# Optimization experiments

Hardware: AMD Instinct MI355X
Metric: run time of the kernel (lower is better)

## Reference

```python
import jax, jax.numpy as jnp
import numpy as np

HIDDEN = 9000
EMBED = 300
STEPS = 20


def _lstm_cell(x, h, c, w_ih, w_hh, b_ih, b_hh):
    # x: [1, in], h/c: [1, H]; gates: [1, 4H] in torch order i, f, g, o
    gates = x @ w_ih.T + b_ih + h @ w_hh.T + b_hh
    i, f, g, o = jnp.split(gates, 4, axis=-1)
    c_new = jax.nn.sigmoid(f) * c + jax.nn.sigmoid(i) * jnp.tanh(g)
    h_new = jax.nn.sigmoid(o) * jnp.tanh(c_new)
    return h_new, c_new


def setup_inputs() -> dict:
    key = jax.random.key(0)
    ks = jax.random.split(key, 7)
    s = 1.0 / np.sqrt(HIDDEN)  # torch LSTMCell/Linear default init scale
    x = jax.random.normal(ks[0], (1, EMBED), dtype=jnp.float32)
    w_ih = jax.random.uniform(ks[1], (4 * HIDDEN, EMBED), jnp.float32, -s, s)
    w_hh = jax.random.uniform(ks[2], (4 * HIDDEN, HIDDEN), jnp.float32, -s, s)
    b_ih = jax.random.uniform(ks[3], (4 * HIDDEN,), jnp.float32, -s, s)
    b_hh = jax.random.uniform(ks[4], (4 * HIDDEN,), jnp.float32, -s, s)
    w_out = jax.random.uniform(ks[5], (EMBED, HIDDEN), jnp.float32, -s, s)
    b_out = jax.random.uniform(ks[6], (EMBED,), jnp.float32, -s, s)
    return {"x": x, "w_ih": w_ih, "w_hh": w_hh, "b_ih": b_ih,
            "b_hh": b_hh, "w_out": w_out, "b_out": b_out}


def reference(x, w_ih, w_hh, b_ih, b_hh, w_out, b_out):
    h = jnp.zeros((1, HIDDEN), dtype=x.dtype)
    c = jnp.zeros((1, HIDDEN), dtype=x.dtype)
    # priming step: feed the image/word embedding once
    h, c = _lstm_cell(x, h, c, w_ih, w_hh, b_ih, b_hh)

    def step(carry, _):
        h, c = carry
        out = h @ w_out.T + b_out          # [1, EMBED]
        h, c = _lstm_cell(out, h, c, w_ih, w_hh, b_ih, b_hh)
        h = jax.nn.softmax(h, axis=1)      # softmax over hidden dim, as in source
        return (h, c), h[0]

    (_, _), hs = jax.lax.scan(step, (h, c), None, length=STEPS)
    return hs.T  # [HIDDEN, STEPS] == gen_cap[:, 1:]
```

## Files before the change

### kernel.cpp

```cpp
#include <hip/hip_runtime.h>
#include <hip/hip_fp16.h>
#include <math.h>

#define HID 9000
#define EMB 300
#define NSTEPS 20
#define RS 9216
#define HID8 1125
#define EMB4 75
#define F4_ROW 2250
#define QROW_DW 1152
#define QHALF 576
#define Q_D    1.4054567378526131e-3f
#define Q_INVD 711.5124735378853f

__device__ __forceinline__ float sigmoidf_(float v) {
    return 1.0f / (1.0f + expf(-v));
}

__device__ __forceinline__ float waveReduceSum(float v) {
#pragma unroll
    for (int off = 32; off > 0; off >>= 1) v += __shfl_down(v, off, 64);
    return v;
}

#define I4DOT8(d, v0, v1, aA, aB)                                      \
    {   unsigned int _d = (d);                                         \
        aA = fmaf((float)(((int)(_d << 28)) >> 28), v0.x, aA);         \
        aB = fmaf((float)(((int)(_d << 24)) >> 28), v0.y, aB);         \
        aA = fmaf((float)(((int)(_d << 20)) >> 28), v0.z, aA);         \
        aB = fmaf((float)(((int)(_d << 16)) >> 28), v0.w, aB);         \
        aA = fmaf((float)(((int)(_d << 12)) >> 28), v1.x, aA);         \
        aB = fmaf((float)(((int)(_d <<  8)) >> 28), v1.y, aB);         \
        aA = fmaf((float)(((int)(_d <<  4)) >> 28), v1.z, aA);         \
        aB = fmaf((float)(((int)(_d      )) >> 28), v1.w, aB); }

__device__ __forceinline__ unsigned int quant4(float v) {
    int q = (int)rintf(v * Q_INVD);
    q = q < -8 ? -8 : (q > 7 ? 7 : q);
    return (unsigned int)(q & 0xF);
}

__global__ __launch_bounds__(256) void f32_to_f16_kernel(
    const float* __restrict__ src, __half* __restrict__ dst, int n8)
{
    int i = blockIdx.x * blockDim.x + threadIdx.x;
    const int stride = gridDim.x * blockDim.x;
    const float4* __restrict__ s4 = (const float4*)src;
    float4* __restrict__ d4 = (float4*)dst;
    for (; i < n8; i += stride) {
        float4 a = s4[2 * i];
        float4 b = s4[2 * i + 1];
        float4 o;
        ((__half2*)&o)[0] = __floats2half2_rn(a.x, a.y);
        ((__half2*)&o)[1] = __floats2half2_rn(a.z, a.w);
        ((__half2*)&o)[2] = __floats2half2_rn(b.x, b.y);
        ((__half2*)&o)[3] = __floats2half2_rn(b.z, b.w);
        d4[i] = o;
    }
}

__global__ __launch_bounds__(256) void prime_kernel_h(
    const float* __restrict__ x, const __half* __restrict__ w_ih,
    const float* __restrict__ b_ih, const float* __restrict__ b_hh,
    float* __restrict__ h, float* __restrict__ c, float* __restrict__ hist)
{
    const int j = blockIdx.x;
    const int wave = threadIdx.x >> 6;
    const int lane = threadIdx.x & 63;
    const int row = j + wave * HID;
    const float2* __restrict__ wr = (const float2*)(w_ih + (size_t)row * EMB);
    const float4* __restrict__ x4 = (const float4*)x;
    float acc = 0.0f;
    for (int k = lane; k < EMB4; k += 64) {
        float2 wv = wr[k];
        const __half2* wh = (const __half2*)&wv;
        float2 w0 = __half22float2(wh[0]);
        float2 w1 = __half22float2(wh[1]);
        float4 xv = x4[k];
        acc = fmaf(w0.x, xv.x, acc);
        acc = fmaf(w0.y, xv.y, acc);
        acc = fmaf(w1.x, xv.z, acc);
        acc = fmaf(w1.y, xv.w, acc);
    }
    acc = waveReduceSum(acc);
    __shared__ float gl[4];
    if (lane == 0) gl[wave] = acc + b_ih[row] + b_hh[row];
    __syncthreads();
    if (threadIdx.x == 0) {
        float gi = gl[0], gg = gl[2], go = gl[3];
        float cn = sigmoidf_(gi) * tanhf(gg);
        float hn = sigmoidf_(go) * tanhf(cn);
        c[j] = cn;
        h[j] = hn;
    }
    if (blockIdx.x == 0 && threadIdx.x < RS - HID) h[HID + threadIdx.x] = 0.0f;
    if (blockIdx.x >= 1 && blockIdx.x <= NSTEPS && threadIdx.x < RS - HID)
        hist[(size_t)(blockIdx.x - 1) * RS + HID + threadIdx.x] = 0.0f;
}

__global__ __launch_bounds__(256) void outvec_kernel_h(
    const float* __restrict__ h, const __half* __restrict__ w_out,
    const float* __restrict__ b_out, float* __restrict__ ovec, float sOverride)
{
    const int i = blockIdx.x;
    const float4* __restrict__ wr = (const float4*)(w_out + (size_t)i * HID);
    const float4* __restrict__ h4 = (const float4*)h;
    const bool selfS = sOverride <= 0.0f;
    float acc = 0.0f, se = 0.0f;
    for (int k = threadIdx.x; k < HID8; k += 256) {
        float4 wv = wr[k];
        const __half2* wh = (const __half2*)&wv;
        float4 ha = h4[2 * k];
        float4 hb = h4[2 * k + 1];
        if (selfS)
            se += ((ha.x + ha.y) + (ha.z + ha.w)) + ((hb.x + hb.y) + (hb.z + hb.w));
        float2 w0 = __half22float2(wh[0]);
        float2 w1 = __half22float2(wh[1]);
        float2 w2 = __half22float2(wh[2]);
        float2 w3 = __half22float2(wh[3]);
        acc = fmaf(w0.x, ha.x, acc);
        acc = fmaf(w0.y, ha.y, acc);
        acc = fmaf(w1.x, ha.z, acc);
        acc = fmaf(w1.y, ha.w, acc);
        acc = fmaf(w2.x, hb.x, acc);
        acc = fmaf(w2.y, hb.y, acc);
        acc = fmaf(w3.x, hb.z, acc);
        acc = fmaf(w3.y, hb.w, acc);
    }
    acc = waveReduceSum(acc);
    se = waveReduceSum(se);
    __shared__ float r1[4], r2[4];
    const int wave = threadIdx.x >> 6;
    const int lane = threadIdx.x & 63;
    if (lane == 0) { r1[wave] = acc; r2[wave] = se; }
    __syncthreads();
    if (threadIdx.x == 0) {
        float S = selfS ? ((r2[0] + r2[1]) + (r2[2] + r2[3])) : sOverride;
        ovec[i] = ((r1[0] + r1[1]) + (r1[2] + r1[3])) / S + b_out[i];
    }
}

__global__ __launch_bounds__(256) void convgates_q4(
    const float* __restrict__ h, const float* __restrict__ ovec,
    const float* __restrict__ w_hh, unsigned int* __restrict__ whh4,
    const __half* __restrict__ w_ih,
    const float* __restrict__ b_ih, const float* __restrict__ b_hh,
    float* __restrict__ c, float* __restrict__ e_out)
{
    const int j = blockIdx.x;
    const int wave = threadIdx.x >> 6;
    const int lane = threadIdx.x & 63;
    const int row = j + wave * HID;

    const float4* __restrict__ w4 = (const float4*)(w_hh + (size_t)row * HID);
    unsigned int* __restrict__ dst = whh4 + (size_t)row * QROW_DW;
    const float4* __restrict__ h4 = (const float4*)h;
    float acc = 0.0f;
    for (int it = 0; it < 18; ++it) {
        const int ci = it * 64 + lane;
        unsigned int pack = 0u;
        if (ci < HID8) {
            float4 a = w4[2 * ci];
            float4 b = w4[2 * ci + 1];
            float4 ha = h4[2 * ci];
            float4 hb = h4[2 * ci + 1];
            acc = fmaf(a.x, ha.x, acc);
            acc = fmaf(a.y, ha.y, acc);
            acc = fmaf(a.z, ha.z, acc);
            acc = fmaf(a.w, ha.w, acc);
            acc = fmaf(b.x, hb.x, acc);
            acc = fmaf(b.y, hb.y, acc);
            acc = fmaf(b.z, hb.z, acc);
            acc = fmaf(b.w, hb.w, acc);
            pack = quant4(a.x)
                 | (quant4(a.y) << 4)
                 | (quant4(a.z) << 8)
                 | (quant4(a.w) << 12)
                 | (quant4(b.x) << 16)
                 | (quant4(b.y) << 20)
                 | (quant4(b.z) << 24)
                 | (quant4(b.w) << 28);
        }
        dst[ci] = pack;
    }
    const float2* __restrict__ wir = (const float2*)(w_ih + (size_t)row * EMB);
    const float4* __restrict__ o4 = (const float4*)ovec;
    for (int k = lane; k < EMB4; k += 64) {
        float2 wv = wir[k];
        const __half2* wh = (const __half2*)&wv;
        float2 w0 = __half22float2(wh[0]);
        float2 w1 = __half22float2(wh[1]);
        float4 ov = o4[k];
        acc = fmaf(w0.x, ov.x, acc);
        acc = fmaf(w0.y, ov.y, acc);
        acc = fmaf(w1.x, ov.z, acc);
        acc = fmaf(w1.y, ov.w, acc);
    }
    acc = waveReduceSum(acc);
    __shared__ float gl[4];
    if (lane == 0) gl[wave] = acc + b_ih[row] + b_hh[row];
    __syncthreads();
    if (threadIdx.x == 0) {
        float gi = gl[0], gf = gl[1], gg = gl[2], go = gl[3];
        float cp = c[j];
        float cn = sigmoidf_(gf) * cp + sigmoidf_(gi) * tanhf(gg);
        float hn = sigmoidf_(go) * tanhf(cn);
        c[j] = cn;
        e_out[j] = expf(hn);
    }
}

__global__ __launch_bounds__(256) void gates_q4s2(
    const float* __restrict__ e_in, const float* __restrict__ ovec,
    const unsigned int* __restrict__ whh4, const __half* __restrict__ w_ih,
    const float* __restrict__ b_ih, const float* __restrict__ b_hh,
    float* __restrict__ c, float* __restrict__ e_out,
    float* __restrict__ Svec, int tm1)
{
    const int j0 = blockIdx.x * 2;
    const int wave = threadIdx.x >> 6;
    const int lane = threadIdx.x & 63;
    const int pair = wave >> 1;
    const int half = wave & 1;

    const unsigned int* __restrict__ wpA0 =
        whh4 + (size_t)(j0 + 2 * pair * HID) * QROW_DW;
    const unsigned int* __restrict__ wpB0 = wpA0 + (size_t)HID * QROW_DW;
    const unsigned int* __restrict__ wpA1 = wpA0 + QROW_DW;
    const unsigned int* __restrict__ wpB1 = wpB0 + QROW_DW;
    const float4* __restrict__ e4 = (const float4*)e_in;

    float pA0a = 0.0f, pA0b = 0.0f, pB0a = 0.0f, pB0b = 0.0f;
    float pA1a = 0.0f, pA1b = 0.0f, pB1a = 0.0f, pB1b = 0.0f;
    float se = 0.0f;
    const int base = half * QHALF;
#pragma unroll 3
    for (int it = 0; it < 9; ++it) {
        const int ci = base + it * 64 + lane;
        unsigned int dA0 = wpA0[ci];
        unsigned int dB0 = wpB0[ci];
        unsigned int dA1 = wpA1[ci];
        unsigned int dB1 = wpB1[ci];
        float4 ev0 = e4[2 * ci];
        float4 ev1 = e4[2 * ci + 1];
        if (pair == 0)
            se += ((ev0.x + ev0.y) + (ev0.z + ev0.w))
                + ((ev1.x + ev1.y) + (ev1.z + ev1.w));
        I4DOT8(dA0, ev0, ev1, pA0a, pA0b);
        I4DOT8(dB0, ev0, ev1, pB0a, pB0b);
        I4DOT8(dA1, ev0, ev1, pA1a, pA1b);
        I4DOT8(dB1, ev0, ev1, pB1a, pB1b);
    }
    float pA0 = pA0a + pA0b;
    float pB0 = pB0a + pB0b;
    float pA1 = pA1a + pA1b;
    float pB1 = pB1a + pB1b;

    const int row0 = j0 + wave * HID;
    float ai0 = 0.0f, ai1 = 0.0f;
    const float2* __restrict__ wir0 = (const float2*)(w_ih + (size_t)row0 * EMB);
    const float2* __restrict__ wir1 = wir0 + EMB / 2;
    const float4* __restrict__ o4 = (const float4*)ovec;
    for (int k = lane; k < EMB4; k += 64) {
        float4 ov = o4[k];
        float2 wv0 = wir0[k];
        float2 wv1 = wir1[k];
        const __half2* wh0 = (const __half2*)&wv0;
        const __half2* wh1 = (const __half2*)&wv1;
        float2 a0 = __half22float2(wh0[0]);
        float2 a1 = __half22float2(wh0[1]);
        float2 b0 = __half22float2(wh1[0]);
        float2 b1 = __half22float2(wh1[1]);
        ai0 = fmaf(a0.x, ov.x, ai0);
        ai0 = fmaf(a0.y, ov.y, ai0);
        ai0 = fmaf(a1.x, ov.z, ai0);
        ai0 = fmaf(a1.y, ov.w, ai0);
        ai1 = fmaf(b0.x, ov.x, ai1);
        ai1 = fmaf(b0.y, ov.y, ai1);
        ai1 = fmaf(b1.x, ov.z, ai1);
        ai1 = fmaf(b1.y, ov.w, ai1);
    }

    pA0 = waveReduceSum(pA0);
    pB0 = waveReduceSum(pB0);
    pA1 = waveReduceSum(pA1);
    pB1 = waveReduceSum(pB1);
    ai0 = waveReduceSum(ai0);
    ai1 = waveReduceSum(ai1);
    if (pair == 0) se = waveReduceSum(se);

    __shared__ float gq[4][2][2];
    __shared__ float gih[4][2];
    __shared__ float sp[2];
    if (lane == 0) {
        gq[wave][0][0] = pA0; gq[wave][0][1] = pB0;
        gq[wave][1][0] = pA1; gq[wave][1][1] = pB1;
        gih[wave][0] = ai0 + b_ih[row0] + b_hh[row0];
        gih[wave][1] = ai1 + b_ih[row0 + 1] + b_hh[row0 + 1];
        if (pair == 0) sp[half] = se;
    }
    __syncthreads();
    if (threadIdx.x < 2) {
        const int jj = threadIdx.x;
        const int j = j0 + jj;
        const float S = sp[0] + sp[1];
        const float scale = Q_D / S;
        float gi = (gq[0][jj][0] + gq[1][jj][0]) * scale + gih[0][jj];
        float gf = (gq[0][jj][1] + gq[1][jj][1]) * scale + gih[1][jj];
        float gg = (gq[2][jj][0] + gq[3][jj][0]) * scale + gih[2][jj];
        float go = (gq[2][jj][1] + gq[3][jj][1]) * scale + gih[3][jj];
        float cp = c[j];
        float cn = sigmoidf_(gf) * cp + sigmoidf_(gi) * tanhf(gg);
        float hn = sigmoidf_(go) * tanhf(cn);
        c[j] = cn;
        e_out[j] = expf(hn);
        if (blockIdx.x == 0 && jj == 0) Svec[tm1] = S;
    }
}

__global__ __launch_bounds__(1024) void final_kernel(
    const float* __restrict__ hist, const float* __restrict__ Svec,
    float* __restrict__ outp)
{
    __shared__ float red[16];
    __shared__ float invSl[NSTEPS];
    const int tid = threadIdx.x;
    const int wave = tid >> 6;
    const int lane = tid & 63;

    float s = 0.0f;
    for (int k = tid; k < HID; k += 1024) s += hist[(size_t)(NSTEPS - 1) * RS + k];
    s = waveReduceSum(s);
    if (lane == 0) red[wave] = s;
    __syncthreads();
    if (tid == 0) {
        float s19 = 0.0f;
        for (int i = 0; i < 16; i++) s19 += red[i];
        red[0] = s19;
    }
    __syncthreads();
    if (tid < NSTEPS) invSl[tid] = 1.0f / ((tid == NSTEPS - 1) ? red[0] : Svec[tid]);
    __syncthreads();

    for (int k = tid; k < HID; k += 1024) {
        float o[NSTEPS];
#pragma unroll
        for (int t = 0; t < NSTEPS; t++) o[t] = hist[(size_t)t * RS + k] * invSl[t];
        float4* dst = (float4*)(outp + (size_t)k * NSTEPS);
#pragma unroll
        for (int q = 0; q < 5; q++)
            dst[q] = make_float4(o[4 * q], o[4 * q + 1], o[4 * q + 2], o[4 * q + 3]);
    }
}

__global__ __launch_bounds__(256) void gates_kernel_h(
    const float* __restrict__ h, const float* __restrict__ ovec,
    const __half* __restrict__ w_hh, const __half* __restrict__ w_ih,
    const float* __restrict__ b_ih, const float* __restrict__ b_hh,
    float* __restrict__ c, float* __restrict__ h_raw)
{
    const int j = blockIdx.x;
    const int wave = threadIdx.x >> 6;
    const int lane = threadIdx.x & 63;
    const int row = j + wave * HID;

    const float4* __restrict__ wr = (const float4*)(w_hh + (size_t)row * HID);
    const float4* __restrict__ h4 = (const float4*)h;
    float acc = 0.0f;
    for (int k = lane; k < HID8; k += 64) {
        float4 wv = wr[k];
        const __half2* wh = (const __half2*)&wv;
        float4 ha = h4[2 * k];
        float4 hb = h4[2 * k + 1];
        float2 w0 = __half22float2(wh[0]);
        float2 w1 = __half22float2(wh[1]);
        float2 w2 = __half22float2(wh[2]);
        float2 w3 = __half22float2(wh[3]);
        acc = fmaf(w0.x, ha.x, acc);
        acc = fmaf(w0.y, ha.y, acc);
        acc = fmaf(w1.x, ha.z, acc);
        acc = fmaf(w1.y, ha.w, acc);
        acc = fmaf(w2.x, hb.x, acc);
        acc = fmaf(w2.y, hb.y, acc);
        acc = fmaf(w3.x, hb.z, acc);
        acc = fmaf(w3.y, hb.w, acc);
    }
    const float2* __restrict__ wir = (const float2*)(w_ih + (size_t)row * EMB);
    const float4* __restrict__ o4 = (const float4*)ovec;
    for (int k = lane; k < EMB4; k += 64) {
        float2 wv = wir[k];
        const __half2* wh = (const __half2*)&wv;
        float2 w0 = __half22float2(wh[0]);
        float2 w1 = __half22float2(wh[1]);
        float4 ov = o4[k];
        acc = fmaf(w0.x, ov.x, acc);
        acc = fmaf(w0.y, ov.y, acc);
        acc = fmaf(w1.x, ov.z, acc);
        acc = fmaf(w1.y, ov.w, acc);
    }
    acc = waveReduceSum(acc);
    __shared__ float gl[4];
    if (lane == 0) gl[wave] = acc + b_ih[row] + b_hh[row];
    __syncthreads();
    if (threadIdx.x == 0) {
        float gi = gl[0], gf = gl[1], gg = gl[2], go = gl[3];
        float cp = c[j];
        float cn = sigmoidf_(gf) * cp + sigmoidf_(gi) * tanhf(gg);
        float hn = sigmoidf_(go) * tanhf(cn);
        c[j] = cn;
        h_raw[j] = hn;
    }
}

__global__ __launch_bounds__(256) void prime_kernel(
    const float* __restrict__ x, const float* __restrict__ w_ih,
    const float* __restrict__ b_ih, const float* __restrict__ b_hh,
    float* __restrict__ h, float* __restrict__ c)
{
    const int j = blockIdx.x;
    const int wave = threadIdx.x >> 6;
    const int lane = threadIdx.x & 63;
    const int row = j + wave * HID;
    const float4* __restrict__ wr = (const float4*)(w_ih + (size_t)row * EMB);
    const float4* __restrict__ x4 = (const float4*)x;
    float acc = 0.0f;
    for (int k = lane; k < EMB / 4; k += 64) {
        float4 w = wr[k];
        float4 xv = x4[k];
        acc = fmaf(w.x, xv.x, acc);
        acc = fmaf(w.y, xv.y, acc);
        acc = fmaf(w.z, xv.z, acc);
        acc = fmaf(w.w, xv.w, acc);
    }
    acc = waveReduceSum(acc);
    __shared__ float gl[4];
    if (lane == 0) gl[wave] = acc + b_ih[row] + b_hh[row];
    __syncthreads();
    if (threadIdx.x == 0) {
        float gi = gl[0], gg = gl[2], go = gl[3];
        float cn = sigmoidf_(gi) * tanhf(gg);
        float hn = sigmoidf_(go) * tanhf(cn);
        c[j] = cn;
        h[j] = hn;
    }
    if (blockIdx.x == 0 && threadIdx.x < RS - HID) h[HID + threadIdx.x] = 0.0f;
}

__global__ __launch_bounds__(256) void outvec_kernel(
    const float* __restrict__ h, const float* __restrict__ w_out,
    const float* __restrict__ b_out, float* __restrict__ ovec)
{
    const int i = blockIdx.x;
    const float4* __restrict__ wr = (const float4*)(w_out + (size_t)i * HID);
    const float4* __restrict__ h4 = (const float4*)h;
    float acc = 0.0f;
    for (int k = threadIdx.x; k < HID / 4; k += 256) {
        float4 w = wr[k];
        float4 hv = h4[k];
        acc = fmaf(w.x, hv.x, acc);
        acc = fmaf(w.y, hv.y, acc);
        acc = fmaf(w.z, hv.z, acc);
        acc = fmaf(w.w, hv.w, acc);
    }
    acc = waveReduceSum(acc);
    __shared__ float red[4];
    const int wave = threadIdx.x >> 6;
    const int lane = threadIdx.x & 63;
    if (lane == 0) red[wave] = acc;
    __syncthreads();
    if (threadIdx.x == 0)
        ovec[i] = red[0] + red[1] + red[2] + red[3] + b_out[i];
}

__global__ __launch_bounds__(256) void gates_kernel(
    const float* __restrict__ h, const float* __restrict__ ovec,
    const float* __restrict__ w_hh, const float* __restrict__ w_ih,
    const float* __restrict__ b_ih, const float* __restrict__ b_hh,
    float* __restrict__ c, float* __restrict__ h_raw)
{
    const int j = blockIdx.x;
    const int wave = threadIdx.x >> 6;
    const int lane = threadIdx.x & 63;
    const int row = j + wave * HID;

    const float4* __restrict__ wr = (const float4*)(w_hh + (size_t)row * HID);
    const float4* __restrict__ h4 = (const float4*)h;
    float acc = 0.0f;
    for (int k = lane; k < HID / 4; k += 64) {
        float4 w = wr[k];
        float4 hv = h4[k];
        acc = fmaf(w.x, hv.x, acc);
        acc = fmaf(w.y, hv.y, acc);
        acc = fmaf(w.z, hv.z, acc);
        acc = fmaf(w.w, hv.w, acc);
    }
    const float4* __restrict__ wir = (const float4*)(w_ih + (size_t)row * EMB);
    const float4* __restrict__ o4 = (const float4*)ovec;
    for (int k = lane; k < EMB / 4; k += 64) {
        float4 w = wir[k];
        float4 ov = o4[k];
        acc = fmaf(w.x, ov.x, acc);
        acc = fmaf(w.y, ov.y, acc);
        acc = fmaf(w.z, ov.z, acc);
        acc = fmaf(w.w, ov.w, acc);
    }
    acc = waveReduceSum(acc);
    __shared__ float gl[4];
    if (lane == 0) gl[wave] = acc + b_ih[row] + b_hh[row];
    __syncthreads();
    if (threadIdx.x == 0) {
        float gi = gl[0], gf = gl[1], gg = gl[2], go = gl[3];
        float cp = c[j];
        float cn = sigmoidf_(gf) * cp + sigmoidf_(gi) * tanhf(gg);
        float hn = sigmoidf_(go) * tanhf(cn);
        c[j] = cn;
        h_raw[j] = hn;
    }
}

__global__ __launch_bounds__(1024) void softmax_kernel(
    const float* __restrict__ h_raw, float* __restrict__ h,
    float* __restrict__ outp, int t)
{
    __shared__ float red[16];
    __shared__ float bcast;
    const int tid = threadIdx.x;
    const int wave = tid >> 6;
    const int lane = tid & 63;

    float m = -INFINITY;
    for (int k = tid; k < HID; k += 1024) m = fmaxf(m, h_raw[k]);
#pragma unroll
    for (int off = 32; off > 0; off >>= 1) m = fmaxf(m, __shfl_down(m, off, 64));
    if (lane == 0) red[wave] = m;
    __syncthreads();
    if (tid == 0) {
        float mm = red[0];
        for (int i = 1; i < 16; i++) mm = fmaxf(mm, red[i]);
        bcast = mm;
    }
    __syncthreads();
    const float M = bcast;

    float s = 0.0f;
    for (int k = tid; k < HID; k += 1024) s += expf(h_raw[k] - M);
    s = waveReduceSum(s);
    if (lane == 0) red[wave] = s;
    __syncthreads();
    if (tid == 0) {
        float ss = 0.0f;
        for (int i = 0; i < 16; i++) ss += red[i];
        bcast = ss;
    }
    __syncthreads();
    const float invS = 1.0f / bcast;

    for (int k = tid; k < HID; k += 1024) {
        float v = expf(h_raw[k] - M) * invS;
        h[k] = v;
        outp[(size_t)k * NSTEPS + t] = v;
    }
    if (tid < RS - HID) h[HID + tid] = 0.0f;
}

extern "C" void kernel_launch(void* const* d_in, const int* in_sizes, int n_in,
                              void* d_out, int out_size, void* d_ws, size_t ws_size,
                              hipStream_t stream)
{
    const float* x     = (const float*)d_in[0];
    const float* w_ih  = (const float*)d_in[1];
    const float* w_hh  = (const float*)d_in[2];
    const float* b_ih  = (const float*)d_in[3];
    const float* b_hh  = (const float*)d_in[4];
    const float* w_out = (const float*)d_in[5];
    const float* b_out = (const float*)d_in[6];
    float* outp = (float*)d_out;

    float* ws = (float*)d_ws;
    float* h0    = ws;
    float* c     = ws + 9216;
    float* ovec  = ws + 18432;
    float* Svec  = ws + 18944;
    float* h_raw = ws + 19072;
    float* hist  = ws + 28288;

    const size_t WHH_E  = (size_t)4 * HID * HID;
    const size_t WIH_E  = (size_t)4 * HID * EMB;
    const size_t WOUT_E = (size_t)EMB * HID;
    const size_t BIG_OFF = 1 << 20;
    const size_t WHH4_BYTES = (size_t)4 * HID * QROW_DW * 4;
    const size_t Q4_BYTES   = BIG_OFF + WHH4_BYTES + 2 * (WIH_E + WOUT_E);
    const size_t FP16_BYTES = BIG_OFF + 2 * (WHH_E + WIH_E + WOUT_E);

    if (ws_size >= Q4_BYTES) {
        unsigned int* whh4 = (unsigned int*)((char*)d_ws + BIG_OFF);
        __half* wih_h  = (__half*)((char*)d_ws + BIG_OFF + WHH4_BYTES);
        __half* wout_h = wih_h + WIH_E;

        f32_to_f16_kernel<<<512, 256, 0, stream>>>(w_ih, wih_h, (int)(WIH_E / 8));
        f32_to_f16_kernel<<<256, 256, 0, stream>>>(w_out, wout_h, (int)(WOUT_E / 8));

        prime_kernel_h<<<HID, 256, 0, stream>>>(x, wih_h, b_ih, b_hh, h0, c, hist);
        outvec_kernel_h<<<EMB, 256, 0, stream>>>(h0, wout_h, b_out, ovec, 1.0f);
        convgates_q4<<<HID, 256, 0, stream>>>(h0, ovec, w_hh, whh4, wih_h,
                                              b_ih, b_hh, c, hist);
        for (int t = 1; t < NSTEPS; ++t) {
            outvec_kernel_h<<<EMB, 256, 0, stream>>>(
                hist + (size_t)(t - 1) * RS, wout_h, b_out, ovec, -1.0f);
            gates_q4s2<<<HID / 2, 256, 0, stream>>>(
                hist + (size_t)(t - 1) * RS, ovec, whh4, wih_h,
                b_ih, b_hh, c, hist + (size_t)t * RS, Svec, t - 1);
        }
        final_kernel<<<1, 1024, 0, stream>>>(hist, Svec, outp);
    } else if (ws_size >= FP16_BYTES) {
        __half* whh_h  = (__half*)((char*)d_ws + BIG_OFF);
        __half* wih_h  = whh_h + WHH_E;
        __half* wout_h = wih_h + WIH_E;

        f32_to_f16_kernel<<<2048, 256, 0, stream>>>(w_hh, whh_h, (int)(WHH_E / 8));
        f32_to_f16_kernel<<<512, 256, 0, stream>>>(w_ih, wih_h, (int)(WIH_E / 8));
        f32_to_f16_kernel<<<256, 256, 0, stream>>>(w_out, wout_h, (int)(WOUT_E / 8));

        prime_kernel_h<<<HID, 256, 0, stream>>>(x, wih_h, b_ih, b_hh, h0, c, hist);
        for (int t = 0; t < NSTEPS; ++t) {
            outvec_kernel_h<<<EMB, 256, 0, stream>>>(h0, wout_h, b_out, ovec, 1.0f);
            gates_kernel_h<<<HID, 256, 0, stream>>>(h0, ovec, whh_h, wih_h,
                                                    b_ih, b_hh, c, h_raw);
            softmax_kernel<<<1, 1024, 0, stream>>>(h_raw, h0, outp, t);
        }
    } else {
        prime_kernel<<<HID, 256, 0, stream>>>(x, w_ih, b_ih, b_hh, h0, c);
        for (int t = 0; t < NSTEPS; ++t) {
            outvec_kernel<<<EMB, 256, 0, stream>>>(h0, w_out, b_out, ovec);
            gates_kernel<<<HID, 256, 0, stream>>>(h0, ovec, w_hh, w_ih,
                                                  b_ih, b_hh, c, h_raw);
            softmax_kernel<<<1, 1024, 0, stream>>>(h_raw, h0, outp, t);
        }
    }
}
```

Measured before the change: 1.218 ms.

## Interleave 4-bit weight rows so gates kernel loads one uint4 per lane

The conversion kernel now writes quantized w_hh in an interleaved layout: for each pair of hidden units and gate pair, the four rows' packed dwords sit together as a uint4. The per-step gates kernel then issues one 16-byte load per lane instead of four separate 4-byte loads from rows far apart. The aim is fewer memory transactions and better coalescing on the weight stream that dominates each step. The conversion kernel is restructured to match, processing two hidden units per block.

```diff
diff --git a/kernel.cpp b/kernel.cpp
--- a/kernel.cpp
+++ b/kernel.cpp
@@ -39,6 +39,27 @@
     int q = (int)rintf(v * Q_INVD);
     q = q < -8 ? -8 : (q > 7 ? 7 : q);
     return (unsigned int)(q & 0xF);
+}
+
+__device__ __forceinline__ unsigned int qdot8(
+    float4 a, float4 b, float4 h0v, float4 h1v, float& acc)
+{
+    acc = fmaf(a.x, h0v.x, acc);
+    acc = fmaf(a.y, h0v.y, acc);
+    acc = fmaf(a.z, h0v.z, acc);
+    acc = fmaf(a.w, h0v.w, acc);
+    acc = fmaf(b.x, h1v.x, acc);
+    acc = fmaf(b.y, h1v.y, acc);
+    acc = fmaf(b.z, h1v.z, acc);
+    acc = fmaf(b.w, h1v.w, acc);
+    return quant4(a.x)
+         | (quant4(a.y) << 4)
+         | (quant4(a.z) << 8)
+         | (quant4(a.w) << 12)
+         | (quant4(b.x) << 16)
+         | (quant4(b.y) << 20)
+         | (quant4(b.z) << 24)
+         | (quant4(b.w) << 28);
 }
 
 __global__ __launch_bounds__(256) void f32_to_f16_kernel(
@@ -141,121 +162,45 @@
     }
 }
 
-__global__ __launch_bounds__(256) void convgates_q4(
+__global__ __launch_bounds__(256) void convgates_q4i(
     const float* __restrict__ h, const float* __restrict__ ovec,
-    const float* __restrict__ w_hh, unsigned int* __restrict__ whh4,
+    const float* __restrict__ w_hh, uint4* __restrict__ whh4i,
     const __half* __restrict__ w_ih,
     const float* __restrict__ b_ih, const float* __restrict__ b_hh,
     float* __restrict__ c, float* __restrict__ e_out)
 {
-    const int j = blockIdx.x;
-    const int wave = threadIdx.x >> 6;
-    const int lane = threadIdx.x & 63;
-    const int row = j + wave * HID;
-
-    const float4* __restrict__ w4 = (const float4*)(w_hh + (size_t)row * HID);
-    unsigned int* __restrict__ dst = whh4 + (size_t)row * QROW_DW;
+    const int jp = blockIdx.x;
+    const int j0 = jp * 2;
+    const int wave = threadIdx.x >> 6;
+    const int lane = threadIdx.x & 63;
+    const int pair = wave >> 1;
+    const int half = wave & 1;
+
+    const float4* __restrict__ wA0 =
+        (const float4*)(w_hh + (size_t)(2 * pair * HID + j0) * HID);
+    const float4* __restrict__ wA1 = wA0 + F4_ROW;
+    const float4* __restrict__ wB0 =
+        (const float4*)(w_hh + (size_t)((2 * pair + 1) * HID + j0) * HID);
+    const float4* __restrict__ wB1 = wB0 + F4_ROW;
+    uint4* __restrict__ dst = whh4i + (size_t)(jp * 2 + pair) * QROW_DW;
     const float4* __restrict__ h4 = (const float4*)h;
-    float acc = 0.0f;
-    for (int it = 0; it < 18; ++it) {
-        const int ci = it * 64 + lane;
-        unsigned int pack = 0u;
+
+    float aA0 = 0.0f, aA1 = 0.0f, aB0 = 0.0f, aB1 = 0.0f;
+    const int base = half * QHALF;
+    for (int it = 0; it < 9; ++it) {
+        const int ci = base + it * 64 + lane;
+        uint4 pack;
+        pack.x = pack.y = pack.z = pack.w = 0u;
         if (ci < HID8) {
-            float4 a = w4[2 * ci];
-            float4 b = w4[2 * ci + 1];
-            float4 ha = h4[2 * ci];
-            float4 hb = h4[2 * ci + 1];
-            acc = fmaf(a.x, ha.x, acc);
-            acc = fmaf(a.y, ha.y, acc);
-            acc = fmaf(a.z, ha.z, acc);
-            acc = fmaf(a.w, ha.w, acc);
-            acc = fmaf(b.x, hb.x, acc);
-            acc = fmaf(b.y, hb.y, acc);
-            acc = fmaf(b.z, hb.z, acc);
-            acc = fmaf(b.w, hb.w, acc);
-            pack = quant4(a.x)
-                 | (quant4(a.y) << 4)
-                 | (quant4(a.z) << 8)
-                 | (quant4(a.w) << 12)
-                 | (quant4(b.x) << 16)
-                 | (quant4(b.y) << 20)
-                 | (quant4(b.z) << 24)
-                 | (quant4(b.w) << 28);
+            float4 hv0 = h4[2 * ci];
+            float4 hv1 = h4[2 * ci + 1];
+            pack.x = qdot8(wA0[2 * ci], wA0[2 * ci + 1], hv0, hv1, aA0);
+            pack.y = qdot8(wA1[2 * ci], wA1[2 * ci + 1], hv0, hv1, aA1);
+            pack.z = qdot8(wB0[2 * ci], wB0[2 * ci + 1], hv0, hv1, aB0);
+            pack.w = qdot8(wB1[2 * ci], wB1[2 * ci + 1], hv0, hv1, aB1);
         }
         dst[ci] = pack;
     }
-    const float2* __restrict__ wir = (const float2*)(w_ih + (size_t)row * EMB);
-    const float4* __restrict__ o4 = (const float4*)ovec;
-    for (int k = lane; k < EMB4; k += 64) {
-        float2 wv = wir[k];
-        const __half2* wh = (const __half2*)&wv;
-        float2 w0 = __half22float2(wh[0]);
-        float2 w1 = __half22float2(wh[1]);
-        float4 ov = o4[k];
-        acc = fmaf(w0.x, ov.x, acc);
-        acc = fmaf(w0.y, ov.y, acc);
-        acc = fmaf(w1.x, ov.z, acc);
-        acc = fmaf(w1.y, ov.w, acc);
-    }
-    acc = waveReduceSum(acc);
-    __shared__ float gl[4];
-    if (lane == 0) gl[wave] = acc + b_ih[row] + b_hh[row];
-    __syncthreads();
-    if (threadIdx.x == 0) {
-        float gi = gl[0], gf = gl[1], gg = gl[2], go = gl[3];
-        float cp = c[j];
-        float cn = sigmoidf_(gf) * cp + sigmoidf_(gi) * tanhf(gg);
-        float hn = sigmoidf_(go) * tanhf(cn);
-        c[j] = cn;
-        e_out[j] = expf(hn);
-    }
-}
-
-__global__ __launch_bounds__(256) void gates_q4s2(
-    const float* __restrict__ e_in, const float* __restrict__ ovec,
-    const unsigned int* __restrict__ whh4, const __half* __restrict__ w_ih,
-    const float* __restrict__ b_ih, const float* __restrict__ b_hh,
-    float* __restrict__ c, float* __restrict__ e_out,
-    float* __restrict__ Svec, int tm1)
-{
-    const int j0 = blockIdx.x * 2;
-    const int wave = threadIdx.x >> 6;
-    const int lane = threadIdx.x & 63;
-    const int pair = wave >> 1;
-    const int half = wave & 1;
-
-    const unsigned int* __restrict__ wpA0 =
-        whh4 + (size_t)(j0 + 2 * pair * HID) * QROW_DW;
-    const unsigned int* __restrict__ wpB0 = wpA0 + (size_t)HID * QROW_DW;
-    const unsigned int* __restrict__ wpA1 = wpA0 + QROW_DW;
-    const unsigned int* __restrict__ wpB1 = wpB0 + QROW_DW;
-    const float4* __restrict__ e4 = (const float4*)e_in;
-
-    float pA0a = 0.0f, pA0b = 0.0f, pB0a = 0.0f, pB0b = 0.0f;
-    float pA1a = 0.0f, pA1b = 0.0f, pB1a = 0.0f, pB1b = 0.0f;
-    float se = 0.0f;
-    const int base = half * QHALF;
-#pragma unroll 3
-    for (int it = 0; it < 9; ++it) {
-        const int ci = base + it * 64 + lane;
-        unsigned int dA0 = wpA0[ci];
-        unsigned int dB0 = wpB0[ci];
-        unsigned int dA1 = wpA1[ci];
-        unsigned int dB1 = wpB1[ci];
-        float4 ev0 = e4[2 * ci];
-        float4 ev1 = e4[2 * ci + 1];
-        if (pair == 0)
-            se += ((ev0.x + ev0.y) + (ev0.z + ev0.w))
-                + ((ev1.x + ev1.y) + (ev1.z + ev1.w));
-        I4DOT8(dA0, ev0, ev1, pA0a, pA0b);
-        I4DOT8(dB0, ev0, ev1, pB0a, pB0b);
-        I4DOT8(dA1, ev0, ev1, pA1a, pA1b);
-        I4DOT8(dB1, ev0, ev1, pB1a, pB1b);
-    }
-    float pA0 = pA0a + pA0b;
-    float pB0 = pB0a + pB0b;
-    float pA1 = pA1a + pA1b;
-    float pB1 = pB1a + pB1b;
 
     const int row0 = j0 + wave * HID;
     float ai0 = 0.0f, ai1 = 0.0f;
@@ -282,9 +227,105 @@
         ai1 = fmaf(b1.y, ov.w, ai1);
     }
 
+    aA0 = waveReduceSum(aA0);
+    aA1 = waveReduceSum(aA1);
+    aB0 = waveReduceSum(aB0);
+    aB1 = waveReduceSum(aB1);
+    ai0 = waveReduceSum(ai0);
+    ai1 = waveReduceSum(ai1);
+
+    __shared__ float gq[4][2][2];
+    __shared__ float gih[4][2];
+    if (lane == 0) {
+        gq[wave][0][0] = aA0; gq[wave][0][1] = aB0;
+        gq[wave][1][0] = aA1; gq[wave][1][1] = aB1;
+        gih[wave][0] = ai0 + b_ih[row0] + b_hh[row0];
+        gih[wave][1] = ai1 + b_ih[row0 + 1] + b_hh[row0 + 1];
+    }
+    __syncthreads();
+    if (threadIdx.x < 2) {
+        const int jj = threadIdx.x;
+        const int j = j0 + jj;
+        float gi = (gq[0][jj][0] + gq[1][jj][0]) + gih[0][jj];
+        float gf = (gq[0][jj][1] + gq[1][jj][1]) + gih[1][jj];
+        float gg = (gq[2][jj][0] + gq[3][jj][0]) + gih[2][jj];
+        float go = (gq[2][jj][1] + gq[3][jj][1]) + gih[3][jj];
+        float cp = c[j];
+        float cn = sigmoidf_(gf) * cp + sigmoidf_(gi) * tanhf(gg);
+        float hn = sigmoidf_(go) * tanhf(cn);
+        c[j] = cn;
+        e_out[j] = expf(hn);
+    }
+}
+
+__global__ __launch_bounds__(256) void gates_q4i(
+    const float* __restrict__ e_in, const float* __restrict__ ovec,
+    const uint4* __restrict__ whh4i, const __half* __restrict__ w_ih,
+    const float* __restrict__ b_ih, const float* __restrict__ b_hh,
+    float* __restrict__ c, float* __restrict__ e_out,
+    float* __restrict__ Svec, int tm1)
+{
+    const int jp = blockIdx.x;
+    const int j0 = jp * 2;
+    const int wave = threadIdx.x >> 6;
+    const int lane = threadIdx.x & 63;
+    const int pair = wave >> 1;
+    const int half = wave & 1;
+
+    const uint4* __restrict__ wp = whh4i + (size_t)(jp * 2 + pair) * QROW_DW;
+    const float4* __restrict__ e4 = (const float4*)e_in;
+
+    float pA0a = 0.0f, pA0b = 0.0f, pA1a = 0.0f, pA1b = 0.0f;
+    float pB0a = 0.0f, pB0b = 0.0f, pB1a = 0.0f, pB1b = 0.0f;
+    float se = 0.0f;
+    const int base = half * QHALF;
+#pragma unroll 3
+    for (int it = 0; it < 9; ++it) {
+        const int ci = base + it * 64 + lane;
+        uint4 wv = wp[ci];
+        float4 ev0 = e4[2 * ci];
+        float4 ev1 = e4[2 * ci + 1];
+        if (pair == 0)
+            se += ((ev0.x + ev0.y) + (ev0.z + ev0.w))
+                + ((ev1.x + ev1.y) + (ev1.z + ev1.w));
+        I4DOT8(wv.x, ev0, ev1, pA0a, pA0b);
+        I4DOT8(wv.y, ev0, ev1, pA1a, pA1b);
+        I4DOT8(wv.z, ev0, ev1, pB0a, pB0b);
+        I4DOT8(wv.w, ev0, ev1, pB1a, pB1b);
+    }
+    float pA0 = pA0a + pA0b;
+    float pA1 = pA1a + pA1b;
+    float pB0 = pB0a + pB0b;
+    float pB1 = pB1a + pB1b;
+
+    const int row0 = j0 + wave * HID;
+    float ai0 = 0.0f, ai1 = 0.0f;
+    const float2* __restrict__ wir0 = (const float2*)(w_ih + (size_t)row0 * EMB);
+    const float2* __restrict__ wir1 = wir0 + EMB / 2;
+    const float4* __restrict__ o4 = (const float4*)ovec;
+    for (int k = lane; k < EMB4; k += 64) {
+        float4 ov = o4[k];
+        float2 wv0 = wir0[k];
+        float2 wv1 = wir1[k];
+        const __half2* wh0 = (const __half2*)&wv0;
+        const __half2* wh1 = (const __half2*)&wv1;
+        float2 a0 = __half22float2(wh0[0]);
+        float2 a1 = __half22float2(wh0[1]);
+        float2 b0 = __half22float2(wh1[0]);
+        float2 b1 = __half22float2(wh1[1]);
+        ai0 = fmaf(a0.x, ov.x, ai0);
+        ai0 = fmaf(a0.y, ov.y, ai0);
+        ai0 = fmaf(a1.x, ov.z, ai0);
+        ai0 = fmaf(a1.y, ov.w, ai0);
+        ai1 = fmaf(b0.x, ov.x, ai1);
+        ai1 = fmaf(b0.y, ov.y, ai1);
+        ai1 = fmaf(b1.x, ov.z, ai1);
+        ai1 = fmaf(b1.y, ov.w, ai1);
+    }
+
     pA0 = waveReduceSum(pA0);
+    pA1 = waveReduceSum(pA1);
     pB0 = waveReduceSum(pB0);
-    pA1 = waveReduceSum(pA1);
     pB1 = waveReduceSum(pB1);
     ai0 = waveReduceSum(ai0);
     ai1 = waveReduceSum(ai1);
@@ -594,7 +635,7 @@
     const size_t FP16_BYTES = BIG_OFF + 2 * (WHH_E + WIH_E + WOUT_E);
 
     if (ws_size >= Q4_BYTES) {
-        unsigned int* whh4 = (unsigned int*)((char*)d_ws + BIG_OFF);
+        uint4* whh4i  = (uint4*)((char*)d_ws + BIG_OFF);
         __half* wih_h  = (__half*)((char*)d_ws + BIG_OFF + WHH4_BYTES);
         __half* wout_h = wih_h + WIH_E;
 
@@ -603,13 +644,13 @@
 
         prime_kernel_h<<<HID, 256, 0, stream>>>(x, wih_h, b_ih, b_hh, h0, c, hist);
         outvec_kernel_h<<<EMB, 256, 0, stream>>>(h0, wout_h, b_out, ovec, 1.0f);
-        convgates_q4<<<HID, 256, 0, stream>>>(h0, ovec, w_hh, whh4, wih_h,
-                                              b_ih, b_hh, c, hist);
+        convgates_q4i<<<HID / 2, 256, 0, stream>>>(h0, ovec, w_hh, whh4i, wih_h,
+                                                   b_ih, b_hh, c, hist);
         for (int t = 1; t < NSTEPS; ++t) {
             outvec_kernel_h<<<EMB, 256, 0, stream>>>(
                 hist + (size_t)(t - 1) * RS, wout_h, b_out, ovec, -1.0f);
-            gates_q4s2<<<HID / 2, 256, 0, stream>>>(
-                hist + (size_t)(t - 1) * RS, ovec, whh4, wih_h,
+            gates_q4i<<<HID / 2, 256, 0, stream>>>(
+                hist + (size_t)(t - 1) * RS, ovec, whh4i, wih_h,
                 b_ih, b_hh, c, hist + (size_t)t * RS, Svec, t - 1);
         }
         final_kernel<<<1, 1024, 0, stream>>>(hist, Svec, outp);
```

Result: faster. 1.187 ms (-2.5%).
